# Optimization experiments

Measured on AMD Instinct MI355X. Metric: run time of the kernel, lower is better.

Reference implementation:

```python
import jax, jax.numpy as jnp
import numpy as np
from jax import lax

N_FILTERS = 256
N_ITER = 20
N_HISTORY = 4
N_CLASSES = 100
BITS = 8            # n_bits_activ passed to Quan_layer
POOL_FREQ = 5
EPS = 1e-5


def quantize_ste(w, bits):
    # Uniform symmetric quantization to `bits` with straight-through estimator.
    n = 2.0 ** (bits - 1) - 1.0
    s = jnp.max(jnp.abs(w)) / n
    q = jnp.round(w / s) * s
    return w + lax.stop_gradient(q - w)


def max_pool2(x):
    return lax.reduce_window(x, -jnp.inf, lax.max, (1, 1, 2, 2), (1, 1, 2, 2), 'VALID')


def setup_inputs() -> dict:
    key = jax.random.key(0)
    ks = jax.random.split(key, 5)
    x = jax.random.normal(ks[0], (16, 3, 64, 64), jnp.float32)
    conv_w = jax.random.normal(ks[1], (N_FILTERS, N_FILTERS, 3, 3), jnp.float32) / np.sqrt(9.0 * N_FILTERS).astype(np.float32)
    alpha = jnp.zeros((N_ITER, N_HISTORY + 1), jnp.float32)
    alpha = alpha.at[:, 0].set(0.1).at[:, 1].set(0.9)
    alpha = alpha + 0.01 * jax.random.normal(ks[2], (N_ITER, N_HISTORY + 1), jnp.float32)
    bn_gamma = jnp.ones((N_ITER, N_FILTERS), jnp.float32)
    bn_beta = jnp.zeros((N_ITER, N_FILTERS), jnp.float32)
    out_w = jax.random.normal(ks[3], (N_CLASSES, N_FILTERS), jnp.float32) / np.sqrt(float(N_FILTERS)).astype(np.float32)
    out_b = jnp.zeros((N_CLASSES,), jnp.float32)
    return {'x': x, 'conv_w': conv_w, 'alpha': alpha, 'bn_gamma': bn_gamma,
            'bn_beta': bn_beta, 'out_w': out_w, 'out_b': out_b}


def reference(x, conv_w, alpha, bn_gamma, bn_beta, out_w, out_b):
    pool_at = [t % POOL_FREQ == POOL_FREQ - 1 for t in range(N_ITER)]
    c_in = x.shape[1]
    # zero-pad channels up to n_filters (F.pad on dim 1)
    x = jnp.pad(x, ((0, 0), (0, N_FILTERS - c_in), (0, 0), (0, 0)))
    hist = [None] * (N_HISTORY - 1) + [x]
    wq = quantize_ste(conv_w, BITS)  # shared quantized conv weight
    for t in range(N_ITER):
        a = lax.conv_general_dilated(hist[-1], wq, (1, 1), ((1, 1), (1, 1)),
                                     dimension_numbers=('NCHW', 'OIHW', 'NCHW'))
        a = jax.nn.relu(a)
        a = alpha[t, 0] * a
        for i, h in enumerate(hist):
            if h is not None:
                a = a + alpha[t, i + 1] * h
        # BatchNorm2d (training-mode batch stats, biased variance)
        mean = jnp.mean(a, axis=(0, 2, 3), keepdims=True)
        var = jnp.var(a, axis=(0, 2, 3), keepdims=True)
        a = (a - mean) / jnp.sqrt(var + EPS)
        a = a * bn_gamma[t][None, :, None, None] + bn_beta[t][None, :, None, None]
        # faithful shift: hist[0] is never overwritten (stays None)
        hist = [hist[0]] + hist[2:] + [a]
        if pool_at[t]:
            hist = [None if h is None else max_pool2(h) for h in hist]
    out = jnp.max(hist[-1], axis=(2, 3))  # adaptive_max_pool2d -> (1,1)
    return out @ out_w.T + out_b
```

## Files before the change

kernel.cpp:

```cpp
#include <hip/hip_runtime.h>
#include <hip/hip_fp16.h>
#include <cstddef>
#include <cstdint>


#define NB 16
#define NIT 20

typedef _Float16 half8 __attribute__((ext_vector_type(8)));
typedef _Float16 half4v __attribute__((ext_vector_type(4)));
typedef float floatx4 __attribute__((ext_vector_type(4)));

__device__ __forceinline__ void gl_lds16(const void* g, void* l) {
  __builtin_amdgcn_global_load_lds(
      (const __attribute__((address_space(1))) unsigned int*)g,
      (__attribute__((address_space(3))) unsigned int*)l, 16, 0, 0);
}

template <int N>
__device__ __forceinline__ void wait_vm() {
  if constexpr (N == 0) asm volatile("s_waitcnt vmcnt(0)" ::: "memory");
  else if constexpr (N == 5) asm volatile("s_waitcnt vmcnt(5)" ::: "memory");
  else if constexpr (N == 6) asm volatile("s_waitcnt vmcnt(6)" ::: "memory");
  else static_assert(N == 0 || N == 5 || N == 6, "add vmcnt literal");
}

__global__ void wmax_part_kernel(const float* __restrict__ w, float* __restrict__ part, int n) {
  float m = 0.f;
  for (int i = blockIdx.x * blockDim.x + threadIdx.x; i < n; i += gridDim.x * blockDim.x)
    m = fmaxf(m, fabsf(w[i]));
  #pragma unroll
  for (int o = 32; o > 0; o >>= 1) m = fmaxf(m, __shfl_down(m, o));
  __shared__ float sm[4];
  int wid = threadIdx.x >> 6, lane = threadIdx.x & 63;
  if (lane == 0) sm[wid] = m;
  __syncthreads();
  if (threadIdx.x == 0) part[blockIdx.x] = fmaxf(fmaxf(sm[0], sm[1]), fmaxf(sm[2], sm[3]));
}

__global__ void wmax_final_kernel(const float* __restrict__ part, float* __restrict__ sout) {
  float m = part[threadIdx.x];
  #pragma unroll
  for (int o = 32; o > 0; o >>= 1) m = fmaxf(m, __shfl_down(m, o));
  __shared__ float sm[4];
  int wid = threadIdx.x >> 6, lane = threadIdx.x & 63;
  if (lane == 0) sm[wid] = m;
  __syncthreads();
  if (threadIdx.x == 0) sout[0] = fmaxf(fmaxf(sm[0], sm[1]), fmaxf(sm[2], sm[3])) / 127.f;
}

__global__ void quant_kernel(const float* __restrict__ w, const float* __restrict__ sptr,
                             _Float16* __restrict__ wqr, int nw) {
  int d = blockIdx.x * 256 + threadIdx.x;
  if (d >= nw) return;
  int frag = d >> 9;
  int e = d & 511;
  int l = e >> 3, j = e & 7;
  int tap = frag >> 7;
  int rem = frag & 127;
  int cog = rem >> 3, chk = rem & 7;
  int co = cog * 16 + (l & 15);
  int ci = chk * 32 + (l >> 4) * 8 + j;
  float s = sptr[0];
  float q = rintf(w[((size_t)co * 256 + ci) * 9 + tap] / s) * s;
  wqr[d] = (_Float16)q;
}

__global__ void pad_kernel(const float* __restrict__ x, _Float16* __restrict__ out) {
  int idx = blockIdx.x * 256 + threadIdx.x;
  int c = idx & 255;
  int pos = idx >> 8;
  int hw = pos & 4095;
  int n = pos >> 12;
  float v = 0.f;
  if (c < 3) v = x[(n * 3 + c) * 4096 + hw];
  out[idx] = (_Float16)v;
}

template <int S, int R>
__global__ __launch_bounds__(512, 2) void conv_mfma_v7(
    const _Float16* __restrict__ in, const _Float16* __restrict__ wqr,
    const float* __restrict__ alpha, int t,
    const _Float16* h1, const _Float16* __restrict__ h2,
    const _Float16* __restrict__ h3, _Float16* pre,
    const _Float16* __restrict__ zpage,
    float* __restrict__ psum, float* __restrict__ psum2) {
  constexpr int NT = 512;
  constexpr int LW = S + 2;
  constexpr int XSLOT = (R + 2) * LW * 4;
  constexpr int XI = (XSLOT + NT - 1) / NT;
  constexpr int XPAD = XI * NT;
  constexpr int WSLOT = 36 * 64;
  constexpr int WI = (WSLOT + NT - 1) / NT;
  constexpr int WPAD = WI * NT;
  static_assert(R * S == 512, "block pixel tile must be 512");

  __shared__ half8 xl[2][XPAD];
  __shared__ half8 wl[WPAD];

  const int tid = threadIdx.x;
  const int lane = tid & 63;
  const int wid = tid >> 6;
  const int l16 = lane & 15;
  const int kg = lane >> 4;
  const int wn = wid;

  constexpr int BPI = S / R;
  const int n = blockIdx.x / BPI;
  const int rb = blockIdx.x % BPI;
  const int cob = blockIdx.y * 64;

  const _Float16* img = in + (size_t)n * S * S * 256;

  int rg[4], cg[4];
  #pragma unroll
  for (int g = 0; g < 4; ++g) {
    int lp = wn * 64 + g * 16 + l16;
    rg[g] = lp / S;
    cg[g] = lp - rg[g] * S;
  }

  floatx4 acc[4][4];
  #pragma unroll
  for (int f = 0; f < 4; ++f)
    #pragma unroll
    for (int g = 0; g < 4; ++g)
      acc[f][g] = (floatx4){0.f, 0.f, 0.f, 0.f};

  auto stageX = [&](int buf, int c) {
    const _Float16* cbase = img + c * 32;
    #pragma unroll
    for (int i = 0; i < XI; ++i) {
      int slot = i * NT + tid;
      const void* g = (const void*)zpage;
      if (slot < XSLOT) {
        int pix = slot >> 2;
        int cig = (slot & 3) ^ ((pix >> 1) & 3);
        int hp = pix / LW, wp = pix - hp * LW;
        int h = rb * R + hp - 1, w = wp - 1;
        if ((unsigned)h < (unsigned)S && (unsigned)w < (unsigned)S)
          g = (const void*)(cbase + (size_t)(h * S + w) * 256 + cig * 8);
      }
      gl_lds16(g, (void*)&xl[buf][slot]);
    }
  };

  auto stageW = [&](int c) {
    #pragma unroll
    for (int i = 0; i < WI; ++i) {
      int slot = i * NT + tid;
      const void* g = (const void*)zpage;
      if (slot < WSLOT) {
        int fb = slot >> 6;
        int tap = fb >> 2, f = fb & 3;
        int ll = slot & 63;
        g = (const void*)(wqr +
            ((((size_t)tap * 16 + blockIdx.y * 4 + f) * 8 + c) << 9) + ll * 8);
      }
      gl_lds16(g, (void*)&wl[slot]);
    }
  };

  auto compute = [&](const half8* xb) {
    #pragma unroll
    for (int tap = 0; tap < 9; ++tap) {
      const int dh = tap / 3 - 1;
      const int dw = tap - (tap / 3) * 3 - 1;
      half8 af[4];
      #pragma unroll
      for (int f = 0; f < 4; ++f)
        af[f] = wl[(tap * 4 + f) * 64 + lane];
      half8 bf[4];
      #pragma unroll
      for (int g = 0; g < 4; ++g) {
        int xp = (rg[g] + 1 + dh) * LW + (cg[g] + 1 + dw);
        bf[g] = xb[xp * 4 + (kg ^ ((xp >> 1) & 3))];
      }
      #pragma unroll
      for (int f = 0; f < 4; ++f)
        #pragma unroll
        for (int g = 0; g < 4; ++g)
          acc[f][g] = __builtin_amdgcn_mfma_f32_16x16x32_f16(af[f], bf[g], acc[f][g], 0, 0, 0);
    }
  };

  stageX(0, 0);
  stageW(0);
  wait_vm<0>();
  __builtin_amdgcn_sched_barrier(0);
  __builtin_amdgcn_s_barrier();
  __builtin_amdgcn_sched_barrier(0);

  #pragma unroll
  for (int c = 0; c < 8; ++c) {
    if (c < 7) stageX((c + 1) & 1, c + 1);
    if (c > 0) {
      if (c < 7) wait_vm<XI>();
      else wait_vm<0>();
      __builtin_amdgcn_sched_barrier(0);
      __builtin_amdgcn_s_barrier();
      __builtin_amdgcn_sched_barrier(0);
    }
    compute(&xl[c & 1][0]);
    __builtin_amdgcn_sched_barrier(0);
    __builtin_amdgcn_s_barrier();
    __builtin_amdgcn_sched_barrier(0);
    if (c < 7) stageW(c + 1);
  }

  const float a0 = alpha[t * 5 + 0];
  const float a1 = alpha[t * 5 + 2];
  const float a2 = alpha[t * 5 + 3];
  const float a3 = alpha[t * 5 + 4];
  float ss[4][4], s2v[4][4];
  #pragma unroll
  for (int f = 0; f < 4; ++f)
    #pragma unroll
    for (int r = 0; r < 4; ++r) { ss[f][r] = 0.f; s2v[f][r] = 0.f; }

  const size_t pixbase = (size_t)n * S * S + (size_t)rb * (R * S);
  #pragma unroll
  for (int f = 0; f < 4; ++f) {
    const int co = cob + f * 16 + kg * 4;
    #pragma unroll
    for (int g = 0; g < 4; ++g) {
      int lp = wn * 64 + g * 16 + l16;
      size_t idx = (pixbase + lp) * 256 + co;
      half4v v3 = *(const half4v*)(h3 + idx);
      half4v v1 = {}, v2 = {};
      if (h1) v1 = *(const half4v*)(h1 + idx);
      if (h2) v2 = *(const half4v*)(h2 + idx);
      half4v o;
      #pragma unroll
      for (int r = 0; r < 4; ++r) {
        float pv = a0 * fmaxf(acc[f][g][r], 0.f) + a3 * (float)v3[r];
        if (h1) pv += a1 * (float)v1[r];
        if (h2) pv += a2 * (float)v2[r];
        o[r] = (_Float16)pv;
        ss[f][r] += pv;
        s2v[f][r] += pv * pv;
      }
      *(half4v*)(pre + idx) = o;
    }
  }

  float* sred = reinterpret_cast<float*>(&wl[0]);
  #pragma unroll
  for (int f = 0; f < 4; ++f)
    #pragma unroll
    for (int r = 0; r < 4; ++r) {
      float a = ss[f][r], b = s2v[f][r];
      #pragma unroll
      for (int m = 1; m < 16; m <<= 1) {
        a += __shfl_xor(a, m);
        b += __shfl_xor(b, m);
      }
      if (l16 == 0) {
        sred[wn * 64 + f * 16 + kg * 4 + r] = a;
        sred[512 + wn * 64 + f * 16 + kg * 4 + r] = b;
      }
    }
  __syncthreads();
  if (tid < 64) {
    float a = 0.f, b = 0.f;
    #pragma unroll
    for (int w = 0; w < 8; ++w) {
      a += sred[w * 64 + tid];
      b += sred[512 + w * 64 + tid];
    }
    psum[(size_t)blockIdx.x * 256 + cob + tid] = a;
    psum2[(size_t)blockIdx.x * 256 + cob + tid] = b;
  }
}

template <int S, int R>
__global__ __launch_bounds__(512, 2) void conv_mfma_sm(
    const _Float16* __restrict__ in, const _Float16* __restrict__ wqr,
    const float* __restrict__ alpha, int t,
    const _Float16* h1, const _Float16* __restrict__ h2,
    const _Float16* __restrict__ h3, _Float16* pre,
    const _Float16* __restrict__ zpage,
    float* __restrict__ psum, float* __restrict__ psum2) {
  constexpr int LW = S + 2;
  constexpr int PIX = (R + 2) * LW;
  constexpr int XS = PIX * 4;
  constexpr int XS_PAD = ((XS + 63) / 64) * 64;
  constexpr int WS = 36 * 64;
  constexpr int PIXB = R * S;
  constexpr int G = PIXB / 64;

  __shared__ half8 xl[2][XS_PAD];
  __shared__ half8 wl[2][WS];
  __shared__ float sred[8][4][2][4];
  __shared__ float sredq[8][4][2][4];

  const int tid = threadIdx.x;
  const int lane = tid & 63;
  const int wid = tid >> 6;
  const int l16 = lane & 15;
  const int kg = lane >> 4;
  const int wm = wid >> 2;
  const int wn = wid & 3;

  constexpr int BPI = S / R;
  const int n = blockIdx.x / BPI;
  const int rb = blockIdx.x % BPI;
  const int cob = blockIdx.y * 64;

  const _Float16* img = in + (size_t)n * S * S * 256;

  floatx4 acc[2][G];
  #pragma unroll
  for (int f = 0; f < 2; ++f)
    #pragma unroll
    for (int g = 0; g < G; ++g)
      acc[f][g] = (floatx4){0.f, 0.f, 0.f, 0.f};

  auto stage = [&](int buf, int c) {
    const _Float16* cbase = img + c * 32;
    for (int sb = wid * 64; sb < XS_PAD; sb += 512) {
      int slot = sb + lane;
      const void* g = (const void*)zpage;
      if (slot < XS) {
        int pix = slot >> 2;
        int cig = (slot & 3) ^ ((pix >> 1) & 3);
        int hp = pix / LW, wp = pix - hp * LW;
        int h = rb * R + hp - 1, w = wp - 1;
        if ((unsigned)h < (unsigned)S && (unsigned)w < (unsigned)S)
          g = (const void*)(cbase + (size_t)(h * S + w) * 256 + cig * 8);
      }
      gl_lds16(g, (void*)&xl[buf][sb]);
    }
    for (int fb = wid; fb < 36; fb += 8) {
      int tap = fb >> 2, cogl = fb & 3;
      const _Float16* g = wqr +
          ((((size_t)tap * 16 + blockIdx.y * 4 + cogl) * 8 + c) << 9) + lane * 8;
      gl_lds16((const void*)g, (void*)&wl[buf][fb * 64]);
    }
  };

  auto compute = [&](int buf) {
    #pragma unroll
    for (int dh = -1; dh <= 1; ++dh) {
      #pragma unroll
      for (int dw = -1; dw <= 1; ++dw) {
        const int tap = (dh + 1) * 3 + (dw + 1);
        half8 af[2];
        #pragma unroll
        for (int f = 0; f < 2; ++f)
          af[f] = wl[buf][(tap * 4 + wm * 2 + f) * 64 + lane];
        half8 bf[G];
        #pragma unroll
        for (int g = 0; g < G; ++g) {
          int p = wn * (PIXB / 4) + g * 16 + l16;
          int r = p / S, cc = p - r * S;
          int lp = (r + 1 + dh) * LW + (cc + 1 + dw);
          bf[g] = xl[buf][lp * 4 + (kg ^ ((lp >> 1) & 3))];
        }
        #pragma unroll
        for (int f = 0; f < 2; ++f)
          #pragma unroll
          for (int g = 0; g < G; ++g)
            acc[f][g] = __builtin_amdgcn_mfma_f32_16x16x32_f16(af[f], bf[g], acc[f][g], 0, 0, 0);
      }
    }
  };

  stage(0, 0);
  __syncthreads();
  for (int c = 0; c < 8; ++c) {
    if (c < 7) stage((c + 1) & 1, c + 1);
    compute(c & 1);
    __syncthreads();
  }

  const float a0 = alpha[t * 5 + 0];
  const float a1 = alpha[t * 5 + 2];
  const float a2 = alpha[t * 5 + 3];
  const float a3 = alpha[t * 5 + 4];
  float ss[2][4], sq[2][4];
  #pragma unroll
  for (int f = 0; f < 2; ++f)
    #pragma unroll
    for (int r = 0; r < 4; ++r) { ss[f][r] = 0.f; sq[f][r] = 0.f; }

  const size_t pix0 = (size_t)n * S * S + (size_t)rb * PIXB;
  #pragma unroll
  for (int f = 0; f < 2; ++f) {
    const int co = cob + wm * 32 + f * 16 + kg * 4;
    #pragma unroll
    for (int g = 0; g < G; ++g) {
      int p = wn * (PIXB / 4) + g * 16 + l16;
      size_t idx = (pix0 + p) * 256 + co;
      half4v v3 = *(const half4v*)(h3 + idx);
      half4v v1 = {}, v2 = {};
      if (h1) v1 = *(const half4v*)(h1 + idx);
      if (h2) v2 = *(const half4v*)(h2 + idx);
      half4v o;
      #pragma unroll
      for (int r = 0; r < 4; ++r) {
        float pv = a0 * fmaxf(acc[f][g][r], 0.f) + a3 * (float)v3[r];
        if (h1) pv += a1 * (float)v1[r];
        if (h2) pv += a2 * (float)v2[r];
        o[r] = (_Float16)pv;
        ss[f][r] += pv;
        sq[f][r] += pv * pv;
      }
      *(half4v*)(pre + idx) = o;
    }
  }

  #pragma unroll
  for (int f = 0; f < 2; ++f)
    #pragma unroll
    for (int r = 0; r < 4; ++r) {
      float a = ss[f][r], b = sq[f][r];
      #pragma unroll
      for (int m = 1; m < 16; m <<= 1) {
        a += __shfl_xor(a, m);
        b += __shfl_xor(b, m);
      }
      if (l16 == 0) { sred[wid][kg][f][r] = a; sredq[wid][kg][f][r] = b; }
    }
  __syncthreads();
  if (tid < 64) {
    int ch = tid;
    int wmm = ch >> 5, ff = (ch >> 4) & 1, kk = (ch >> 2) & 3, rr = ch & 3;
    float a = 0.f, b = 0.f;
    #pragma unroll
    for (int w = 0; w < 4; ++w) {
      a += sred[wmm * 4 + w][kk][ff][rr];
      b += sredq[wmm * 4 + w][kk][ff][rr];
    }
    psum[(size_t)blockIdx.x * 256 + cob + ch] = a;
    psum2[(size_t)blockIdx.x * 256 + cob + ch] = b;
  }
}

__global__ void stats_final_kernel(const float* __restrict__ psum, const float* __restrict__ psum2,
                                   const float* __restrict__ gamma, const float* __restrict__ beta,
                                   int t, float M, int nblk,
                                   float* __restrict__ scale, float* __restrict__ shift) {
  int c = blockIdx.x;
  float s = 0.f, s2 = 0.f;
  for (int b = threadIdx.x; b < nblk; b += 64) {
    s += psum[(size_t)b * 256 + c];
    s2 += psum2[(size_t)b * 256 + c];
  }
  #pragma unroll
  for (int o = 32; o > 0; o >>= 1) {
    s += __shfl_down(s, o);
    s2 += __shfl_down(s2, o);
  }
  if (threadIdx.x == 0) {
    float mean = s / M;
    float var = s2 / M - mean * mean;
    float sc = gamma[t * 256 + c] * rsqrtf(var + 1e-5f);
    scale[c] = sc;
    shift[c] = beta[t * 256 + c] - mean * sc;
  }
}

__global__ void apply_kernel(_Float16* __restrict__ x, const float* __restrict__ scale,
                             const float* __restrict__ shift, int n8) {
  int i = blockIdx.x * 256 + threadIdx.x;
  if (i >= n8) return;
  half8 v = *(half8*)(x + (size_t)i * 8);
  int c0 = (i * 8) & 255;
  half8 o;
  #pragma unroll
  for (int j = 0; j < 8; ++j) o[j] = (_Float16)((float)v[j] * scale[c0 + j] + shift[c0 + j]);
  *(half8*)(x + (size_t)i * 8) = o;
}

__global__ void pool3_kernel(const _Float16* __restrict__ s0, const _Float16* __restrict__ s1,
                             const _Float16* __restrict__ s2,
                             _Float16* __restrict__ d0, _Float16* __restrict__ d1,
                             _Float16* __restrict__ d2,
                             const float* __restrict__ scale, const float* __restrict__ shift,
                             int So, int total8) {
  int i = blockIdx.x * 256 + threadIdx.x;
  if (i >= total8) return;
  int z = blockIdx.y;
  const _Float16* in = (z == 0) ? s0 : (z == 1) ? s1 : s2;
  _Float16* out = (z == 0) ? d0 : (z == 1) ? d1 : d2;
  int c0 = (i & 31) * 8;
  int pix = i >> 5;
  int wo = pix % So;
  int t1 = pix / So;
  int ho = t1 % So;
  int n = t1 / So;
  int Si = So * 2;
  size_t b00 = ((size_t)(n * Si * Si) + (2 * ho) * Si + 2 * wo) * 256 + c0;
  half8 v00 = *(const half8*)(in + b00);
  half8 v01 = *(const half8*)(in + b00 + 256);
  half8 v10 = *(const half8*)(in + b00 + (size_t)Si * 256);
  half8 v11 = *(const half8*)(in + b00 + (size_t)Si * 256 + 256);
  half8 o;
  if (z == 2) {
    #pragma unroll
    for (int j = 0; j < 8; ++j) {
      float sc = scale[c0 + j], sh = shift[c0 + j];
      float a = (float)v00[j] * sc + sh;
      float b = (float)v01[j] * sc + sh;
      float c = (float)v10[j] * sc + sh;
      float d = (float)v11[j] * sc + sh;
      o[j] = (_Float16)fmaxf(fmaxf(a, b), fmaxf(c, d));
    }
  } else {
    #pragma unroll
    for (int j = 0; j < 8; ++j) {
      float m = fmaxf(fmaxf((float)v00[j], (float)v01[j]),
                      fmaxf((float)v10[j], (float)v11[j]));
      o[j] = (_Float16)m;
    }
  }
  *(half8*)(out + (size_t)pix * 256 + c0) = o;
}

__global__ void amax_kernel(const _Float16* __restrict__ x, float* __restrict__ vec) {
  int i = blockIdx.x * blockDim.x + threadIdx.x;
  if (i >= NB * 256) return;
  int n = i >> 8, c = i & 255;
  float m = -1e30f;
  for (int p = 0; p < 16; ++p)
    m = fmaxf(m, (float)x[((size_t)(n * 16 + p)) * 256 + c]);
  vec[i] = m;
}

__global__ void linear_kernel(const float* __restrict__ vec, const float* __restrict__ W,
                              const float* __restrict__ b, float* __restrict__ out) {
  int n = blockIdx.x, j = threadIdx.x;
  if (j >= 100) return;
  float s = b[j];
  const float* v = vec + n * 256;
  const float* w = W + j * 256;
  for (int c = 0; c < 256; ++c) s += v[c] * w[c];
  out[n * 100 + j] = s;
}

extern "C" void kernel_launch(void* const* d_in, const int* in_sizes, int n_in,
                              void* d_out, int out_size, void* d_ws, size_t ws_size,
                              hipStream_t stream) {
  const float* x        = (const float*)d_in[0];
  const float* conv_w   = (const float*)d_in[1];
  const float* alpha    = (const float*)d_in[2];
  const float* bn_gamma = (const float*)d_in[3];
  const float* bn_beta  = (const float*)d_in[4];
  const float* out_w    = (const float*)d_in[5];
  const float* out_b    = (const float*)d_in[6];
  float* out = (float*)d_out;

  char* ws = (char*)d_ws;
  size_t off = 0;
  auto alloc = [&](size_t bytes) -> void* {
    void* p = (void*)(ws + off);
    off = (off + bytes + 255) & ~(size_t)255;
    return p;
  };
  const size_t SLAB = (size_t)NB * 4096 * 256 * 2;
  char* slab[4];
  size_t slabsz[4];
  for (int i = 0; i < 3; ++i) { slab[i] = (char*)alloc(SLAB); slabsz[i] = SLAB; }
  slab[3] = (char*)alloc(3 * (SLAB / 4)); slabsz[3] = 3 * (SLAB / 4);
  _Float16* wqr  = (_Float16*)alloc((size_t)9 * 256 * 256 * 2);
  float* wpart = (float*)alloc(256 * 4);
  float* sq    = (float*)alloc(256);
  float* psum  = (float*)alloc(256 * 256 * 4);
  float* psum2 = (float*)alloc(256 * 256 * 4);
  float* scale = (float*)alloc(256 * 4);
  float* shift = (float*)alloc(256 * 4);
  float* vec   = (float*)alloc((size_t)NB * 256 * 4);
  _Float16* zpage = (_Float16*)alloc(256);
  (void)ws_size;

  const int NW = 256 * 256 * 9;

  hipMemsetAsync(zpage, 0, 256, stream);

  hipLaunchKernelGGL(wmax_part_kernel, dim3(256), dim3(256), 0, stream, conv_w, wpart, NW);
  hipLaunchKernelGGL(wmax_final_kernel, dim3(1), dim3(256), 0, stream, wpart, sq);
  hipLaunchKernelGGL(quant_kernel, dim3((NW + 255) / 256), dim3(256), 0, stream, conv_w, sq, wqr, NW);

  hipLaunchKernelGGL(pad_kernel, dim3((NB * 4096 * 256) / 256), dim3(256), 0, stream,
                     x, (_Float16*)slab[0]);

  auto contains = [&](int k, char* p) -> bool {
    return p && p >= slab[k] && p < slab[k] + slabsz[k];
  };

  char *p1 = nullptr, *p2 = nullptr, *p3 = slab[0];
  int S = 64;
  for (int t = 0; t < NIT; ++t) {
    char* dst;
    if (p1) {
      dst = p1;
    } else {
      dst = nullptr;
      for (int k = 0; k < 3; ++k)
        if (!contains(k, p2) && !contains(k, p3)) { dst = slab[k]; break; }
    }
    const _Float16* h1 = (const _Float16*)p1;
    const _Float16* h2 = (const _Float16*)p2;
    const _Float16* h3 = (const _Float16*)p3;
    _Float16* pre = (_Float16*)dst;

    int nblk;
    switch (S) {
      case 64: {
        dim3 grid(NB * 8, 4);  nblk = NB * 8;
        hipLaunchKernelGGL((conv_mfma_v7<64, 8>), grid, dim3(512), 0, stream,
                           h3, wqr, alpha, t, h1, h2, h3, pre, zpage, psum, psum2);
        break;
      }
      case 32: {
        dim3 grid(NB * 2, 4);  nblk = NB * 2;
        hipLaunchKernelGGL((conv_mfma_v7<32, 16>), grid, dim3(512), 0, stream,
                           h3, wqr, alpha, t, h1, h2, h3, pre, zpage, psum, psum2);
        break;
      }
      case 16: {
        dim3 grid(NB * 4, 4);  nblk = NB * 4;
        hipLaunchKernelGGL((conv_mfma_sm<16, 4>), grid, dim3(512), 0, stream,
                           h3, wqr, alpha, t, h1, h2, h3, pre, zpage, psum, psum2);
        break;
      }
      default: {
        dim3 grid(NB * 1, 4);  nblk = NB * 1;
        hipLaunchKernelGGL((conv_mfma_sm<8, 8>), grid, dim3(512), 0, stream,
                           h3, wqr, alpha, t, h1, h2, h3, pre, zpage, psum, psum2);
        break;
      }
    }

    int npix = NB * S * S;
    hipLaunchKernelGGL(stats_final_kernel, dim3(256), dim3(64), 0, stream,
                       psum, psum2, bn_gamma, bn_beta, t, (float)npix, nblk, scale, shift);

    if (t % 5 != 4) {
      int n8 = npix * 32;
      hipLaunchKernelGGL(apply_kernel, dim3((n8 + 255) / 256), dim3(256), 0, stream,
                         pre, scale, shift, n8);
      p1 = p2; p2 = p3; p3 = dst;
    } else {
      char* q1 = p2;
      char* q2 = p3;
      char* q3 = dst;
      int So = S / 2;
      size_t qbytes = (size_t)NB * So * So * 256 * 2;
      char* fs = nullptr;
      for (int k = 0; k < 4; ++k)
        if (!contains(k, q1) && !contains(k, q2) && !contains(k, q3)) { fs = slab[k]; break; }
      int total8 = NB * So * So * 32;
      dim3 pg((total8 + 255) / 256, 3);
      hipLaunchKernelGGL(pool3_kernel, pg, dim3(256), 0, stream,
                         (const _Float16*)q1, (const _Float16*)q2, (const _Float16*)q3,
                         (_Float16*)fs, (_Float16*)(fs + qbytes), (_Float16*)(fs + 2 * qbytes),
                         scale, shift, So, total8);
      p1 = fs; p2 = fs + qbytes; p3 = fs + 2 * qbytes;
      S = So;
    }
  }

  hipLaunchKernelGGL(amax_kernel, dim3(16), dim3(256), 0, stream, (const _Float16*)p3, vec);
  hipLaunchKernelGGL(linear_kernel, dim3(NB), dim3(128), 0, stream, vec, out_w, out_b, out);
}
```

Measured before the change: 1.152 ms.

## Generalize conv tile to wider output-channel blocks and drop column halo

Templates the main MFMA conv kernel on output-channel block width and wave count. At 64x64 each block now covers 128 output channels with waves split 2x4, so each staged input tile feeds twice as many channels and input reloads fall. The LDS tile no longer stores left/right halo columns; out-of-range columns are zeroed in registers at compute time, which removes padding slots and the slot guards in staging. The 32x32 case switches to smaller 256-thread blocks with more blocks. The channel loop is no longer force-unrolled, which adds register/LDS pressure trade-offs and per-tap select overhead.

```diff
diff --git a/kernel.cpp b/kernel.cpp
--- a/kernel.cpp
+++ b/kernel.cpp
@@ -21,8 +21,7 @@
 __device__ __forceinline__ void wait_vm() {
   if constexpr (N == 0) asm volatile("s_waitcnt vmcnt(0)" ::: "memory");
   else if constexpr (N == 5) asm volatile("s_waitcnt vmcnt(5)" ::: "memory");
-  else if constexpr (N == 6) asm volatile("s_waitcnt vmcnt(6)" ::: "memory");
-  else static_assert(N == 0 || N == 5 || N == 6, "add vmcnt literal");
+  else static_assert(N == 0 || N == 5, "add vmcnt literal");
 }
 
 __global__ void wmax_part_kernel(const float* __restrict__ w, float* __restrict__ part, int n) {
@@ -77,54 +76,58 @@
   out[idx] = (_Float16)v;
 }
 
-template <int S, int R>
-__global__ __launch_bounds__(512, 2) void conv_mfma_v7(
+template <int S, int R, int CO_B, int NWAVES>
+__global__ __launch_bounds__(NWAVES * 64, 2) void conv_mfma_v8(
     const _Float16* __restrict__ in, const _Float16* __restrict__ wqr,
     const float* __restrict__ alpha, int t,
     const _Float16* h1, const _Float16* __restrict__ h2,
     const _Float16* __restrict__ h3, _Float16* pre,
     const _Float16* __restrict__ zpage,
     float* __restrict__ psum, float* __restrict__ psum2) {
-  constexpr int NT = 512;
-  constexpr int LW = S + 2;
-  constexpr int XSLOT = (R + 2) * LW * 4;
-  constexpr int XI = (XSLOT + NT - 1) / NT;
-  constexpr int XPAD = XI * NT;
-  constexpr int WSLOT = 36 * 64;
-  constexpr int WI = (WSLOT + NT - 1) / NT;
-  constexpr int WPAD = WI * NT;
-  static_assert(R * S == 512, "block pixel tile must be 512");
-
-  __shared__ half8 xl[2][XPAD];
-  __shared__ half8 wl[WPAD];
+  constexpr int NT = NWAVES * 64;
+  constexpr int XSLOT = (R + 2) * S * 4;
+  constexpr int XI = XSLOT / NT;
+  static_assert(XSLOT % NT == 0, "X issues must be uniform");
+  constexpr int WFR = CO_B / 16;
+  constexpr int WSLOT = 9 * WFR * 64;
+  constexpr int WI = WSLOT / NT;
+  static_assert(WSLOT % NT == 0, "W issues must be uniform");
+  constexpr int WM_N = CO_B / 64;
+  constexpr int WN_N = NWAVES / WM_N;
+  constexpr int WPIX = (R * S) / WN_N;
+  constexpr int G = WPIX / 16;
+
+  __shared__ half8 xl[2][XSLOT];
+  __shared__ half8 wl[WSLOT];
 
   const int tid = threadIdx.x;
   const int lane = tid & 63;
   const int wid = tid >> 6;
   const int l16 = lane & 15;
   const int kg = lane >> 4;
-  const int wn = wid;
-
-  constexpr int BPI = S / R;
+  const int wm = wid / WN_N;
+  const int wn = wid % WN_N;
+
+  constexpr int BPI = (S * S) / (R * S);
   const int n = blockIdx.x / BPI;
   const int rb = blockIdx.x % BPI;
-  const int cob = blockIdx.y * 64;
+  const int cob = blockIdx.y * CO_B;
 
   const _Float16* img = in + (size_t)n * S * S * 256;
 
-  int rg[4], cg[4];
-  #pragma unroll
-  for (int g = 0; g < 4; ++g) {
-    int lp = wn * 64 + g * 16 + l16;
+  int rg[G], cg[G];
+  #pragma unroll
+  for (int g = 0; g < G; ++g) {
+    int lp = wn * WPIX + g * 16 + l16;
     rg[g] = lp / S;
     cg[g] = lp - rg[g] * S;
   }
 
-  floatx4 acc[4][4];
+  floatx4 acc[4][G];
   #pragma unroll
   for (int f = 0; f < 4; ++f)
     #pragma unroll
-    for (int g = 0; g < 4; ++g)
+    for (int g = 0; g < G; ++g)
       acc[f][g] = (floatx4){0.f, 0.f, 0.f, 0.f};
 
   auto stageX = [&](int buf, int c) {
@@ -132,15 +135,13 @@
     #pragma unroll
     for (int i = 0; i < XI; ++i) {
       int slot = i * NT + tid;
+      int pix = slot >> 2;
+      int cig = (slot & 3) ^ ((pix >> 1) & 3);
+      int hp = pix / S, wp = pix - hp * S;
+      int h = rb * R + hp - 1;
       const void* g = (const void*)zpage;
-      if (slot < XSLOT) {
-        int pix = slot >> 2;
-        int cig = (slot & 3) ^ ((pix >> 1) & 3);
-        int hp = pix / LW, wp = pix - hp * LW;
-        int h = rb * R + hp - 1, w = wp - 1;
-        if ((unsigned)h < (unsigned)S && (unsigned)w < (unsigned)S)
-          g = (const void*)(cbase + (size_t)(h * S + w) * 256 + cig * 8);
-      }
+      if ((unsigned)h < (unsigned)S)
+        g = (const void*)(cbase + (size_t)(h * S + wp) * 256 + cig * 8);
       gl_lds16(g, (void*)&xl[buf][slot]);
     }
   };
@@ -149,15 +150,12 @@
     #pragma unroll
     for (int i = 0; i < WI; ++i) {
       int slot = i * NT + tid;
-      const void* g = (const void*)zpage;
-      if (slot < WSLOT) {
-        int fb = slot >> 6;
-        int tap = fb >> 2, f = fb & 3;
-        int ll = slot & 63;
-        g = (const void*)(wqr +
-            ((((size_t)tap * 16 + blockIdx.y * 4 + f) * 8 + c) << 9) + ll * 8);
-      }
-      gl_lds16(g, (void*)&wl[slot]);
+      int fb = slot >> 6;
+      int tap = fb / WFR, fr = fb - tap * WFR;
+      int ll = slot & 63;
+      const _Float16* g = wqr +
+          ((((size_t)tap * 16 + blockIdx.y * WFR + fr) * 8 + c) << 9) + ll * 8;
+      gl_lds16((const void*)g, (void*)&wl[slot]);
     }
   };
 
@@ -169,17 +167,22 @@
       half8 af[4];
       #pragma unroll
       for (int f = 0; f < 4; ++f)
-        af[f] = wl[(tap * 4 + f) * 64 + lane];
-      half8 bf[4];
-      #pragma unroll
-      for (int g = 0; g < 4; ++g) {
-        int xp = (rg[g] + 1 + dh) * LW + (cg[g] + 1 + dw);
-        bf[g] = xb[xp * 4 + (kg ^ ((xp >> 1) & 3))];
+        af[f] = wl[(tap * WFR + wm * 4 + f) * 64 + lane];
+      half8 bf[G];
+      #pragma unroll
+      for (int g = 0; g < G; ++g) {
+        int cw = cg[g] + dw;
+        bool oob = (unsigned)cw >= (unsigned)S;
+        int cs = oob ? cg[g] : cw;
+        int xp = (rg[g] + 1 + dh) * S + cs;
+        half8 b = xb[xp * 4 + (kg ^ ((xp >> 1) & 3))];
+        if (oob) b = (half8){};
+        bf[g] = b;
       }
       #pragma unroll
       for (int f = 0; f < 4; ++f)
         #pragma unroll
-        for (int g = 0; g < 4; ++g)
+        for (int g = 0; g < G; ++g)
           acc[f][g] = __builtin_amdgcn_mfma_f32_16x16x32_f16(af[f], bf[g], acc[f][g], 0, 0, 0);
     }
   };
@@ -191,11 +194,10 @@
   __builtin_amdgcn_s_barrier();
   __builtin_amdgcn_sched_barrier(0);
 
-  #pragma unroll
   for (int c = 0; c < 8; ++c) {
     if (c < 7) stageX((c + 1) & 1, c + 1);
     if (c > 0) {
-      if (c < 7) wait_vm<XI>();
+      if (c < 7) wait_vm<5>();
       else wait_vm<0>();
       __builtin_amdgcn_sched_barrier(0);
       __builtin_amdgcn_s_barrier();
@@ -212,19 +214,25 @@
   const float a1 = alpha[t * 5 + 2];
   const float a2 = alpha[t * 5 + 3];
   const float a3 = alpha[t * 5 + 4];
-  float ss[4][4], s2v[4][4];
+  float ss[4][G], s2v[4][G];
   #pragma unroll
   for (int f = 0; f < 4; ++f)
     #pragma unroll
-    for (int r = 0; r < 4; ++r) { ss[f][r] = 0.f; s2v[f][r] = 0.f; }
+    for (int g = 0; g < G; ++g) { ss[f][g] = 0.f; s2v[f][g] = 0.f; }
+
+  float cs[4][4], cq[4][4];
+  #pragma unroll
+  for (int f = 0; f < 4; ++f)
+    #pragma unroll
+    for (int r = 0; r < 4; ++r) { cs[f][r] = 0.f; cq[f][r] = 0.f; }
 
   const size_t pixbase = (size_t)n * S * S + (size_t)rb * (R * S);
   #pragma unroll
   for (int f = 0; f < 4; ++f) {
-    const int co = cob + f * 16 + kg * 4;
-    #pragma unroll
-    for (int g = 0; g < 4; ++g) {
-      int lp = wn * 64 + g * 16 + l16;
+    const int co = cob + wm * 64 + f * 16 + kg * 4;
+    #pragma unroll
+    for (int g = 0; g < G; ++g) {
+      int lp = wn * WPIX + g * 16 + l16;
       size_t idx = (pixbase + lp) * 256 + co;
       half4v v3 = *(const half4v*)(h3 + idx);
       half4v v1 = {}, v2 = {};
@@ -237,8 +245,8 @@
         if (h1) pv += a1 * (float)v1[r];
         if (h2) pv += a2 * (float)v2[r];
         o[r] = (_Float16)pv;
-        ss[f][r] += pv;
-        s2v[f][r] += pv * pv;
+        cs[f][r] += pv;
+        cq[f][r] += pv * pv;
       }
       *(half4v*)(pre + idx) = o;
     }
@@ -249,24 +257,26 @@
   for (int f = 0; f < 4; ++f)
     #pragma unroll
     for (int r = 0; r < 4; ++r) {
-      float a = ss[f][r], b = s2v[f][r];
+      float a = cs[f][r], b = cq[f][r];
       #pragma unroll
       for (int m = 1; m < 16; m <<= 1) {
         a += __shfl_xor(a, m);
         b += __shfl_xor(b, m);
       }
       if (l16 == 0) {
-        sred[wn * 64 + f * 16 + kg * 4 + r] = a;
-        sred[512 + wn * 64 + f * 16 + kg * 4 + r] = b;
+        sred[wid * 64 + f * 16 + kg * 4 + r] = a;
+        sred[NWAVES * 64 + wid * 64 + f * 16 + kg * 4 + r] = b;
       }
     }
   __syncthreads();
-  if (tid < 64) {
+  if (tid < CO_B) {
+    int half = tid >> 6;
+    int ch = tid & 63;
     float a = 0.f, b = 0.f;
     #pragma unroll
-    for (int w = 0; w < 8; ++w) {
-      a += sred[w * 64 + tid];
-      b += sred[512 + w * 64 + tid];
+    for (int w = 0; w < WN_N; ++w) {
+      a += sred[(half * WN_N + w) * 64 + ch];
+      b += sred[NWAVES * 64 + (half * WN_N + w) * 64 + ch];
     }
     psum[(size_t)blockIdx.x * 256 + cob + tid] = a;
     psum2[(size_t)blockIdx.x * 256 + cob + tid] = b;
@@ -608,14 +618,14 @@
     int nblk;
     switch (S) {
       case 64: {
-        dim3 grid(NB * 8, 4);  nblk = NB * 8;
-        hipLaunchKernelGGL((conv_mfma_v7<64, 8>), grid, dim3(512), 0, stream,
+        dim3 grid(NB * 8, 2);  nblk = NB * 8;
+        hipLaunchKernelGGL((conv_mfma_v8<64, 8, 128, 8>), grid, dim3(512), 0, stream,
                            h3, wqr, alpha, t, h1, h2, h3, pre, zpage, psum, psum2);
         break;
       }
       case 32: {
-        dim3 grid(NB * 2, 4);  nblk = NB * 2;
-        hipLaunchKernelGGL((conv_mfma_v7<32, 16>), grid, dim3(512), 0, stream,
+        dim3 grid(NB * 4, 4);  nblk = NB * 4;
+        hipLaunchKernelGGL((conv_mfma_v8<32, 8, 64, 4>), grid, dim3(256), 0, stream,
                            h3, wqr, alpha, t, h1, h2, h3, pre, zpage, psum, psum2);
         break;
       }
```

Result: slower. 1.837 ms (+59.5%).
